# Kernel tuning notes

Measured on AMD Instinct MI355X. Metric: run time of the kernel, lower is better.

## Reference

```python
import jax, jax.numpy as jnp
import numpy as np

LOW_DIM, SKIP_DIM, OUT_DIM = 512, 256, 256
EPS_IDW = 1e-8
EPS_LN = 1e-5
K = 3


def setup_inputs() -> dict:
    key = jax.random.key(0)
    ks = jax.random.split(key, 10)
    B, N, S = 4, 8192, 2048
    xyz_hi = jax.random.uniform(ks[0], (B, N, 3), dtype=jnp.float32)
    xyz_lo = jax.random.uniform(ks[1], (B, S, 3), dtype=jnp.float32)
    feat_skip = jax.random.normal(ks[2], (B, N, SKIP_DIM), dtype=jnp.float32)
    feat_lo = jax.random.normal(ks[3], (B, S, LOW_DIM), dtype=jnp.float32)
    in_dim = LOW_DIM + SKIP_DIM
    W1 = jax.random.normal(ks[4], (in_dim, OUT_DIM), dtype=jnp.float32) / np.sqrt(in_dim)
    b1 = jnp.zeros((OUT_DIM,), dtype=jnp.float32)
    W2 = jax.random.normal(ks[5], (OUT_DIM, OUT_DIM), dtype=jnp.float32) / np.sqrt(OUT_DIM)
    b2 = jnp.zeros((OUT_DIM,), dtype=jnp.float32)
    gamma = jnp.ones((OUT_DIM,), dtype=jnp.float32)
    beta = jnp.zeros((OUT_DIM,), dtype=jnp.float32)
    return {"xyz_hi": xyz_hi, "xyz_lo": xyz_lo, "feat_skip": feat_skip,
            "feat_lo": feat_lo, "W1": W1, "b1": b1, "W2": W2, "b2": b2,
            "gamma": gamma, "beta": beta}


def _layer_norm(x, gamma, beta):
    mu = jnp.mean(x, axis=-1, keepdims=True)
    var = jnp.mean(jnp.square(x - mu), axis=-1, keepdims=True)
    return (x - mu) * jax.lax.rsqrt(var + EPS_LN) * gamma + beta


def reference(xyz_hi, xyz_lo, feat_skip, feat_lo, W1, b1, W2, b2, gamma, beta):
    B, N, _ = xyz_hi.shape
    _, S, _ = xyz_lo.shape
    if S == 1:
        interpolated = jnp.broadcast_to(feat_lo, (B, N, feat_lo.shape[-1]))
    else:
        # pairwise Euclidean distances: (B, N, S)
        d2 = (jnp.sum(xyz_hi ** 2, -1)[:, :, None]
              + jnp.sum(xyz_lo ** 2, -1)[:, None, :]
              - 2.0 * jnp.einsum('bnd,bsd->bns', xyz_hi, xyz_lo))
        dists = jnp.sqrt(jnp.maximum(d2, 0.0))
        # smallest-3 via top_k on negated distances
        neg_d, knn_idx = jax.lax.top_k(-dists, K)          # (B, N, 3)
        dk = -neg_d
        inv_d = 1.0 / (dk + EPS_IDW)
        weights = inv_d / jnp.sum(inv_d, axis=-1, keepdims=True)  # (B, N, 3)
        # gather neighbor features: (B, N, 3, low_dim)
        knn_feat = feat_lo[jnp.arange(B)[:, None, None], knn_idx]
        interpolated = jnp.einsum('bnk,bnkc->bnc', weights, knn_feat)
    fused = jnp.concatenate([feat_skip, interpolated], axis=-1)   # (B, N, skip+low)
    h = jax.nn.relu(fused @ W1 + b1)
    h = h @ W2 + b2
    return _layer_norm(h, gamma, beta)
```

## Files before the change

### kernel.cpp

```cpp
#include <hip/hip_runtime.h>
#include <hip/hip_bf16.h>
#include <stdint.h>

typedef unsigned short u16;
typedef __attribute__((ext_vector_type(8))) short short8;
typedef __attribute__((ext_vector_type(4))) float f32x4;

#define BB 4
#define NN 8192
#define SS 2048
#define MTOT 32768
#define CSKIP 256
#define CLO 512
#define CIN 768
#define COUT 256

__device__ __forceinline__ u16 f2bf(float f) {
  unsigned u = __float_as_uint(f);
  u += 0x7fffu + ((u >> 16) & 1u);
  return (u16)(u >> 16);
}

__device__ __forceinline__ void gl_lds16(const void* g, void* l) {
  __builtin_amdgcn_global_load_lds(
      (const __attribute__((address_space(1))) void*)g,
      (__attribute__((address_space(3))) void*)l, 16, 0, 0);
}

__device__ __forceinline__ void conv_chunk(const float* s, u16* d) {
  union { u16 a[8]; short8 v; } pk;
#pragma unroll
  for (int i = 0; i < 8; ++i) pk.a[i] = f2bf(s[i]);
  *(short8*)d = pk.v;
}

__global__ __launch_bounds__(1024) void knn_wconv_kernel(
    const float* __restrict__ xyz_hi, const float* __restrict__ xyz_lo,
    const float* __restrict__ W1, const float* __restrict__ W2,
    const float* __restrict__ feat_skip, const float* __restrict__ feat_lo,
    float* __restrict__ wq_g, int* __restrict__ iq_g,
    u16* __restrict__ W1aT, u16* __restrict__ W1bT, u16* __restrict__ W2T,
    u16* __restrict__ FSB, u16* __restrict__ FLB) {
  int blk = blockIdx.x;
  int tid = threadIdx.x;

  if ((blk % 5) == 4) {
    int wtid = (blk / 5) * 1024 + tid;
    for (int t = wtid; t < 1048576; t += 131072) {
      int p = t & 3, r = (t >> 2) & 32767, kc = t >> 17;
      int c = p ^ (r & 3);
      conv_chunk(feat_skip + (size_t)r * CSKIP + kc * 32 + c * 8,
                 FSB + (size_t)t * 8);
    }
    for (int t = wtid; t < 524288; t += 131072) {
      int p = t & 3, r = (t >> 2) & 8191, kc = t >> 15;
      int c = p ^ (r & 3);
      conv_chunk(feat_lo + (size_t)r * CLO + kc * 32 + c * 8,
                 FLB + (size_t)t * 8);
    }
    for (int i = wtid; i < 262144; i += 131072) {
      if (i < 65536) {
        int n = i >> 8, k = i & 255;
        W1aT[i] = f2bf(W1[(size_t)k * COUT + n]);
      } else if (i < 196608) {
        int j = i - 65536;
        int n = j >> 9, k = j & 511;
        W1bT[j] = f2bf(W1[(size_t)(256 + k) * COUT + n]);
      } else {
        int j = i - 196608;
        int n = j >> 8, k = j & 255;
        W2T[j] = f2bf(W2[(size_t)k * COUT + n]);
      }
    }
    return;
  }

  __shared__ float md[16][64][3];
  __shared__ int   mi[16][64][3];

  int kblk = (blk / 5) * 4 + (blk % 5);
  int b = kblk >> 7;
  int wave = tid >> 6, lane = tid & 63;
  int qm = kblk * 64 + lane;
  float qx = xyz_hi[(size_t)qm * 3 + 0];
  float qy = xyz_hi[(size_t)qm * 3 + 1];
  float qz = xyz_hi[(size_t)qm * 3 + 2];

  const float* xl = xyz_lo + (size_t)b * SS * 3;
  int j0 = __builtin_amdgcn_readfirstlane(wave * 128);

  float b0 = 1e30f, b1 = 1e30f, b2 = 1e30f;
  int i0 = -1, i1 = -1, i2 = -1;
#pragma unroll 8
  for (int jj = 0; jj < 128; ++jj) {
    int j = j0 + jj;
    float px = xl[3 * j + 0];
    float py = xl[3 * j + 1];
    float pz = xl[3 * j + 2];
    float dx = px - qx, dy = py - qy, dz = pz - qz;
    float d = fmaf(dx, dx, fmaf(dy, dy, dz * dz));
    bool c0 = d < b0, c1 = d < b1, c2 = d < b2;
    float nb0 = fminf(b0, d);
    float nb1 = __builtin_amdgcn_fmed3f(b0, b1, d);
    float nb2 = __builtin_amdgcn_fmed3f(b1, b2, d);
    int ni0 = c0 ? j : i0;
    int ni1 = c0 ? i0 : (c1 ? j : i1);
    int ni2 = c1 ? i1 : (c2 ? j : i2);
    b0 = nb0; b1 = nb1; b2 = nb2;
    i0 = ni0; i1 = ni1; i2 = ni2;
  }
  md[wave][lane][0] = b0; mi[wave][lane][0] = i0;
  md[wave][lane][1] = b1; mi[wave][lane][1] = i1;
  md[wave][lane][2] = b2; mi[wave][lane][2] = i2;
  __syncthreads();

  if (tid < 64) {
    int q = tid;
    float fb0 = 1e30f, fb1 = 1e30f, fb2 = 1e30f;
    int fi0 = -1, fi1 = -1, fi2 = -1;
    for (int p = 0; p < 16; ++p)
#pragma unroll
      for (int s = 0; s < 3; ++s) {
        float d = md[p][q][s]; int ix = mi[p][q][s];
        if (d < fb2 || (d == fb2 && ix < fi2)) {
          fb2 = d; fi2 = ix;
          if (fb2 < fb1 || (fb2 == fb1 && fi2 < fi1)) {
            float t = fb1; fb1 = fb2; fb2 = t; int ti = fi1; fi1 = fi2; fi2 = ti;
          }
          if (fb1 < fb0 || (fb1 == fb0 && fi1 < fi0)) {
            float t = fb0; fb0 = fb1; fb1 = t; int ti = fi0; fi0 = fi1; fi1 = ti;
          }
        }
      }
    int qm2 = kblk * 64 + q;
    float d0 = sqrtf(fb0), d1 = sqrtf(fb1), d2 = sqrtf(fb2);
    float inv0 = 1.0f / (d0 + 1e-8f);
    float inv1 = 1.0f / (d1 + 1e-8f);
    float inv2 = 1.0f / (d2 + 1e-8f);
    float s = inv0 + inv1 + inv2;
    wq_g[(size_t)qm2 * 3 + 0] = inv0 / s;
    wq_g[(size_t)qm2 * 3 + 1] = inv1 / s;
    wq_g[(size_t)qm2 * 3 + 2] = inv2 / s;
    iq_g[(size_t)qm2 * 3 + 0] = fi0;
    iq_g[(size_t)qm2 * 3 + 1] = fi1;
    iq_g[(size_t)qm2 * 3 + 2] = fi2;
  }
}

__global__ __launch_bounds__(256, 4) void ggemm_kernel(
    const u16* __restrict__ FLB, const u16* __restrict__ W1bT,
    float* __restrict__ G) {
  __shared__ u16 As[2][32 * 32];
  __shared__ u16 Bs[2][128 * 32];
  int tid = threadIdx.x;
  int m0 = (blockIdx.x >> 1) << 5;
  int n0 = (blockIdx.x & 1) << 7;
  int w = tid >> 6, lane = tid & 63;
  int quad = lane >> 4, l16 = lane & 15;

  f32x4 zero = {0.f, 0.f, 0.f, 0.f};
  f32x4 acc[2][2];
#pragma unroll
  for (int tm = 0; tm < 2; ++tm)
#pragma unroll
    for (int tn = 0; tn < 2; ++tn) acc[tm][tn] = zero;

  auto stageA = [&](u16* An, int kc) {
    if (tid < 128)
      gl_lds16((const char*)(FLB + ((size_t)kc * NN + m0) * 32) + tid * 16,
               (char*)An + tid * 16);
  };
  auto stageB = [&](u16* Bn, int kc) {
#pragma unroll
    for (int r = 0; r < 2; ++r) {
      int u = tid + r * 256;
      int nrow = u >> 2, c = u & 3;
      int cg = c ^ (nrow & 3);
      gl_lds16(W1bT + (size_t)(n0 + nrow) * CLO + kc * 32 + cg * 8,
               (char*)Bn + u * 16);
    }
  };

  stageB(Bs[0], 0);
  stageA(As[0], 0);

  for (int kc = 0; kc < 16; ++kc) {
    __syncthreads();
    const u16* Ac = As[kc & 1];
    const u16* Bc = Bs[kc & 1];
    if (kc + 1 < 16) {
      stageB(Bs[(kc + 1) & 1], kc + 1);
      stageA(As[(kc + 1) & 1], kc + 1);
    }

    short8 af[2], bf[2];
#pragma unroll
    for (int t = 0; t < 2; ++t) {
      int rr = t * 16 + l16;
      af[t] = *(const short8*)(Ac + (rr * 4 + (quad ^ (rr & 3))) * 8);
    }
#pragma unroll
    for (int t = 0; t < 2; ++t) {
      int rr = w * 32 + t * 16 + l16;
      bf[t] = *(const short8*)(Bc + (rr * 4 + (quad ^ (rr & 3))) * 8);
    }
#pragma unroll
    for (int tm = 0; tm < 2; ++tm)
#pragma unroll
      for (int tn = 0; tn < 2; ++tn)
        acc[tm][tn] = __builtin_amdgcn_mfma_f32_16x16x32_bf16(af[tm], bf[tn], acc[tm][tn], 0, 0, 0);
  }

#pragma unroll
  for (int tm = 0; tm < 2; ++tm)
#pragma unroll
    for (int tn = 0; tn < 2; ++tn) {
      int col = n0 + w * 32 + tn * 16 + l16;
#pragma unroll
      for (int r = 0; r < 4; ++r) {
        int row = m0 + tm * 16 + quad * 4 + r;
        G[(size_t)row * COUT + col] = acc[tm][tn][r];
      }
    }
}

__global__ __launch_bounds__(256, 2) void gemm12_kernel(
    const u16* __restrict__ FSB, const u16* __restrict__ W1aT,
    const float* __restrict__ b1, const float* __restrict__ G,
    const float* __restrict__ wq_g, const int* __restrict__ iq_g,
    const u16* __restrict__ W2T, const float* __restrict__ b2,
    const float* __restrict__ gamma, const float* __restrict__ beta,
    float* __restrict__ out) {
  __shared__ u16 Hs[64 * 264];
  __shared__ u16 Bs[256 * 32];
  __shared__ u16 Bs2[256 * 32];
  __shared__ u16 As[2][64 * 32];
  __shared__ float swq[192];
  __shared__ int   siq[192];
  __shared__ float red[4][64][2];
  __shared__ float stats[64][2];
  int tid = threadIdx.x;
  int m0 = blockIdx.x << 6;
  int bS = (m0 >> 13) * SS;
  int w = tid >> 6, lane = tid & 63;
  int quad = lane >> 4, l16 = lane & 15;

  if (tid < 192) {
    swq[tid] = wq_g[(size_t)m0 * 3 + tid];
    siq[tid] = iq_g[(size_t)m0 * 3 + tid];
  }

  f32x4 zero = {0.f, 0.f, 0.f, 0.f};
  f32x4 acc[4][4];
#pragma unroll
  for (int tm = 0; tm < 4; ++tm)
#pragma unroll
    for (int tn = 0; tn < 4; ++tn) acc[tm][tn] = zero;

  auto stageA = [&](u16* An, int kc) {
    gl_lds16((const char*)(FSB + ((size_t)kc * MTOT + m0) * 32) + tid * 16,
             (char*)An + tid * 16);
  };

#pragma unroll
  for (int r = 0; r < 4; ++r) {
    int u = tid + r * 256;
    int nrow = u >> 2, c = u & 3;
    int cg = c ^ (nrow & 3);
    gl_lds16(W1aT + (size_t)nrow * CSKIP + cg * 8, (char*)Bs + u * 16);
  }
  stageA(As[0], 0);

  for (int kc = 0; kc < 8; ++kc) {
    __syncthreads();
    const u16* Ac = As[kc & 1];
    u16* Bc = (kc & 1) ? Bs2 : Bs;
    if (kc + 1 < 8) {
      u16* Bn = (kc & 1) ? Bs : Bs2;
#pragma unroll
      for (int r = 0; r < 4; ++r) {
        int u = tid + r * 256;
        int nrow = u >> 2, c = u & 3;
        int cg = c ^ (nrow & 3);
        gl_lds16(W1aT + (size_t)nrow * CSKIP + (kc + 1) * 32 + cg * 8,
                 (char*)Bn + u * 16);
      }
      stageA(As[(kc + 1) & 1], kc + 1);
    }

    short8 af[4], bf[4];
#pragma unroll
    for (int t = 0; t < 4; ++t) {
      int rr = t * 16 + l16;
      af[t] = *(const short8*)(Ac + (rr * 4 + (quad ^ (rr & 3))) * 8);
    }
#pragma unroll
    for (int t = 0; t < 4; ++t) {
      int rr = w * 64 + t * 16 + l16;
      bf[t] = *(const short8*)(Bc + (rr * 4 + (quad ^ (rr & 3))) * 8);
    }
#pragma unroll
    for (int tm = 0; tm < 4; ++tm)
#pragma unroll
      for (int tn = 0; tn < 4; ++tn)
        acc[tm][tn] = __builtin_amdgcn_mfma_f32_16x16x32_bf16(af[tm], bf[tn], acc[tm][tn], 0, 0, 0);
  }

  {
    float bias[4];
#pragma unroll
    for (int tn = 0; tn < 4; ++tn) bias[tn] = b1[w * 64 + tn * 16 + l16];
#pragma unroll
    for (int tm = 0; tm < 4; ++tm)
#pragma unroll
      for (int r = 0; r < 4; ++r) {
        int rl = tm * 16 + quad * 4 + r;
        float w0 = swq[rl * 3 + 0], w1 = swq[rl * 3 + 1], w2 = swq[rl * 3 + 2];
        const float* g0 = G + (size_t)(bS + siq[rl * 3 + 0]) * COUT;
        const float* g1 = G + (size_t)(bS + siq[rl * 3 + 1]) * COUT;
        const float* g2 = G + (size_t)(bS + siq[rl * 3 + 2]) * COUT;
#pragma unroll
        for (int tn = 0; tn < 4; ++tn) {
          int col = w * 64 + tn * 16 + l16;
          float gv = fmaf(w0, g0[col], fmaf(w1, g1[col], w2 * g2[col]));
          float v = acc[tm][tn][r] + bias[tn] + gv;
          v = v > 0.f ? v : 0.f;
          Hs[rl * 264 + col] = f2bf(v);
        }
      }
  }

#pragma unroll
  for (int tm = 0; tm < 4; ++tm)
#pragma unroll
    for (int tn = 0; tn < 4; ++tn) acc[tm][tn] = zero;

  __syncthreads();
#pragma unroll
  for (int r = 0; r < 4; ++r) {
    int u = tid + r * 256;
    int nrow = u >> 2, c = u & 3;
    int cg = c ^ (nrow & 3);
    gl_lds16(W2T + (size_t)nrow * COUT + cg * 8, (char*)Bs + u * 16);
  }
  for (int kc = 0; kc < 8; ++kc) {
    __syncthreads();
    u16* cur = (kc & 1) ? Bs2 : Bs;
    u16* nxt = (kc & 1) ? Bs : Bs2;
    if (kc + 1 < 8) {
#pragma unroll
      for (int r = 0; r < 4; ++r) {
        int u = tid + r * 256;
        int nrow = u >> 2, c = u & 3;
        int cg = c ^ (nrow & 3);
        gl_lds16(W2T + (size_t)nrow * COUT + (kc + 1) * 32 + cg * 8,
                 (char*)nxt + u * 16);
      }
    }
    short8 af[4], bf[4];
#pragma unroll
    for (int t = 0; t < 4; ++t)
      af[t] = *(const short8*)(Hs + (t * 16 + l16) * 264 + kc * 32 + quad * 8);
#pragma unroll
    for (int t = 0; t < 4; ++t) {
      int rr = w * 64 + t * 16 + l16;
      bf[t] = *(const short8*)(cur + (rr * 4 + (quad ^ (rr & 3))) * 8);
    }
#pragma unroll
    for (int tm = 0; tm < 4; ++tm)
#pragma unroll
      for (int tn = 0; tn < 4; ++tn)
        acc[tm][tn] = __builtin_amdgcn_mfma_f32_16x16x32_bf16(af[tm], bf[tn], acc[tm][tn], 0, 0, 0);
  }

  float bias[4], g[4], be[4];
#pragma unroll
  for (int tn = 0; tn < 4; ++tn) {
    int col = w * 64 + tn * 16 + l16;
    bias[tn] = b2[col]; g[tn] = gamma[col]; be[tn] = beta[col];
  }
#pragma unroll
  for (int tm = 0; tm < 4; ++tm)
#pragma unroll
    for (int r = 0; r < 4; ++r) {
      float s = 0.f, sq = 0.f;
#pragma unroll
      for (int tn = 0; tn < 4; ++tn) {
        float v = acc[tm][tn][r] + bias[tn];
        acc[tm][tn][r] = v;
        s += v; sq += v * v;
      }
#pragma unroll
      for (int msk = 1; msk < 16; msk <<= 1) {
        s += __shfl_xor(s, msk);
        sq += __shfl_xor(sq, msk);
      }
      if (l16 == 0) {
        int rl = tm * 16 + quad * 4 + r;
        red[w][rl][0] = s;
        red[w][rl][1] = sq;
      }
    }
  __syncthreads();
  if (tid < 64) {
    float s = red[0][tid][0] + red[1][tid][0] + red[2][tid][0] + red[3][tid][0];
    float sq = red[0][tid][1] + red[1][tid][1] + red[2][tid][1] + red[3][tid][1];
    float mu = s * (1.f / 256.f);
    float var = sq * (1.f / 256.f) - mu * mu;
    stats[tid][0] = mu;
    stats[tid][1] = rsqrtf(var + 1e-5f);
  }
  __syncthreads();
#pragma unroll
  for (int tm = 0; tm < 4; ++tm)
#pragma unroll
    for (int r = 0; r < 4; ++r) {
      int rl = tm * 16 + quad * 4 + r;
      float mu = stats[rl][0], rstd = stats[rl][1];
#pragma unroll
      for (int tn = 0; tn < 4; ++tn) {
        int col = w * 64 + tn * 16 + l16;
        out[(size_t)(m0 + rl) * COUT + col] = (acc[tm][tn][r] - mu) * rstd * g[tn] + be[tn];
      }
    }
}

extern "C" void kernel_launch(void* const* d_in, const int* in_sizes, int n_in,
                              void* d_out, int out_size, void* d_ws, size_t ws_size,
                              hipStream_t stream) {
  const float* xyz_hi    = (const float*)d_in[0];
  const float* xyz_lo    = (const float*)d_in[1];
  const float* feat_skip = (const float*)d_in[2];
  const float* feat_lo   = (const float*)d_in[3];
  const float* W1        = (const float*)d_in[4];
  const float* b1        = (const float*)d_in[5];
  const float* W2        = (const float*)d_in[6];
  const float* b2        = (const float*)d_in[7];
  const float* gamma     = (const float*)d_in[8];
  const float* beta      = (const float*)d_in[9];
  float* out = (float*)d_out;

  char* ws = (char*)d_ws;
  u16*   FSB   = (u16*)(ws + 0);
  u16*   W1aT  = (u16*)(ws + 16777216);
  u16*   W1bT  = (u16*)(ws + 16908288);
  u16*   W2T   = (u16*)(ws + 17170432);
  float* wq_g  = (float*)(ws + 17301504);
  int*   iq_g  = (int*)(ws + 17694720);
  float* G     = (float*)(ws + 18087936);
  u16*   FLB   = (u16*)(ws + 26476544);

  knn_wconv_kernel<<<640, 1024, 0, stream>>>(xyz_hi, xyz_lo, W1, W2,
                                             feat_skip, feat_lo,
                                             wq_g, iq_g, W1aT, W1bT, W2T,
                                             FSB, FLB);
  ggemm_kernel<<<(BB * SS) / 32 * 2, 256, 0, stream>>>(FLB, W1bT, G);
  gemm12_kernel<<<MTOT / 64, 256, 0, stream>>>(FSB, W1aT, b1, G, wq_g, iq_g,
                                               W2T, b2, gamma, beta, out);
}
```

Measured before the change: 182.4 us.

## Fold feature bf16 conversion into KNN blocks, overlapping loads with distance search

```diff
diff --git a/kernel.cpp b/kernel.cpp
--- a/kernel.cpp
+++ b/kernel.cpp
@@ -27,10 +27,12 @@
       (__attribute__((address_space(3))) void*)l, 16, 0, 0);
 }
 
-__device__ __forceinline__ void conv_chunk(const float* s, u16* d) {
+__device__ __forceinline__ void pack_store(u16* d, float4 x0, float4 x1) {
   union { u16 a[8]; short8 v; } pk;
-#pragma unroll
-  for (int i = 0; i < 8; ++i) pk.a[i] = f2bf(s[i]);
+  pk.a[0] = f2bf(x0.x); pk.a[1] = f2bf(x0.y);
+  pk.a[2] = f2bf(x0.z); pk.a[3] = f2bf(x0.w);
+  pk.a[4] = f2bf(x1.x); pk.a[5] = f2bf(x1.y);
+  pk.a[6] = f2bf(x1.z); pk.a[7] = f2bf(x1.w);
   *(short8*)d = pk.v;
 }
 
@@ -44,21 +46,9 @@
   int blk = blockIdx.x;
   int tid = threadIdx.x;
 
-  if ((blk % 5) == 4) {
-    int wtid = (blk / 5) * 1024 + tid;
-    for (int t = wtid; t < 1048576; t += 131072) {
-      int p = t & 3, r = (t >> 2) & 32767, kc = t >> 17;
-      int c = p ^ (r & 3);
-      conv_chunk(feat_skip + (size_t)r * CSKIP + kc * 32 + c * 8,
-                 FSB + (size_t)t * 8);
-    }
-    for (int t = wtid; t < 524288; t += 131072) {
-      int p = t & 3, r = (t >> 2) & 8191, kc = t >> 15;
-      int c = p ^ (r & 3);
-      conv_chunk(feat_lo + (size_t)r * CLO + kc * 32 + c * 8,
-                 FLB + (size_t)t * 8);
-    }
-    for (int i = wtid; i < 262144; i += 131072) {
+  if (blk >= 512) {
+    int base = (blk - 512) * 1024 + tid;
+    for (int i = base; i < 262144; i += 65536) {
       if (i < 65536) {
         int n = i >> 8, k = i & 255;
         W1aT[i] = f2bf(W1[(size_t)k * COUT + n]);
@@ -75,13 +65,25 @@
     return;
   }
 
+  int wtid = blk * 1024 + tid;
+  int t0 = wtid;
+  int p0 = t0 & 3, r0 = (t0 >> 2) & 32767, k0 = t0 >> 17;
+  const float* s0 = feat_skip + (size_t)r0 * CSKIP + k0 * 32 + (p0 ^ (r0 & 3)) * 8;
+  int t1 = wtid + 524288;
+  int p1 = t1 & 3, r1 = (t1 >> 2) & 32767, k1 = t1 >> 17;
+  const float* s1 = feat_skip + (size_t)r1 * CSKIP + k1 * 32 + (p1 ^ (r1 & 3)) * 8;
+  int p2 = wtid & 3, r2 = (wtid >> 2) & 8191, k2 = wtid >> 15;
+  const float* s2 = feat_lo + (size_t)r2 * CLO + k2 * 32 + (p2 ^ (r2 & 3)) * 8;
+  float4 c0a = *(const float4*)s0, c0b = *(const float4*)(s0 + 4);
+  float4 c1a = *(const float4*)s1, c1b = *(const float4*)(s1 + 4);
+  float4 c2a = *(const float4*)s2, c2b = *(const float4*)(s2 + 4);
+
   __shared__ float md[16][64][3];
   __shared__ int   mi[16][64][3];
 
-  int kblk = (blk / 5) * 4 + (blk % 5);
-  int b = kblk >> 7;
+  int b = blk >> 7;
   int wave = tid >> 6, lane = tid & 63;
-  int qm = kblk * 64 + lane;
+  int qm = blk * 64 + lane;
   float qx = xyz_hi[(size_t)qm * 3 + 0];
   float qy = xyz_hi[(size_t)qm * 3 + 1];
   float qz = xyz_hi[(size_t)qm * 3 + 2];
@@ -132,7 +134,7 @@
           }
         }
       }
-    int qm2 = kblk * 64 + q;
+    int qm2 = blk * 64 + q;
     float d0 = sqrtf(fb0), d1 = sqrtf(fb1), d2 = sqrtf(fb2);
     float inv0 = 1.0f / (d0 + 1e-8f);
     float inv1 = 1.0f / (d1 + 1e-8f);
@@ -145,6 +147,10 @@
     iq_g[(size_t)qm2 * 3 + 1] = fi1;
     iq_g[(size_t)qm2 * 3 + 2] = fi2;
   }
+
+  pack_store(FSB + (size_t)t0 * 8, c0a, c0b);
+  pack_store(FSB + (size_t)t1 * 8, c1a, c1b);
+  pack_store(FLB + (size_t)wtid * 8, c2a, c2b);
 }
 
 __global__ __launch_bounds__(256, 4) void ggemm_kernel(
@@ -450,7 +456,7 @@
   float* G     = (float*)(ws + 18087936);
   u16*   FLB   = (u16*)(ws + 26476544);
 
-  knn_wconv_kernel<<<640, 1024, 0, stream>>>(xyz_hi, xyz_lo, W1, W2,
+  knn_wconv_kernel<<<576, 1024, 0, stream>>>(xyz_hi, xyz_lo, W1, W2,
                                              feat_skip, feat_lo,
                                              wq_g, iq_g, W1aT, W1bT, W2T,
                                              FSB, FLB);
```

Measured after the change: 174.3 us. 4.4% less time.
